# Kernel optimization log

Hardware: AMD Instinct MI355X
Metric: run time of the kernel (lower is better)

The kernel has to match this reference:

```python
import math
import jax, jax.numpy as jnp
import numpy as np

B, LQ, LK = 4, 128, 512
EMBED_TIME, NUM_HEADS, INPUT_DIM, HIDDEN_DIM = 128, 8, 64, 256
EK = EMBED_TIME // NUM_HEADS  # per-head time-embedding dim


def setup_inputs() -> dict:
    key = jax.random.key(0)
    ks = jax.random.split(key, 10)
    query = jax.random.normal(ks[0], (B, LQ, EMBED_TIME), dtype=jnp.float32)
    k_in = jax.random.normal(ks[1], (B, LK, EMBED_TIME), dtype=jnp.float32)
    value = jax.random.normal(ks[2], (B, LK, INPUT_DIM), dtype=jnp.float32)
    mask = jax.random.randint(ks[3], (B, LK, INPUT_DIM), 0, 2, dtype=jnp.int32)
    s_t = 1.0 / math.sqrt(EMBED_TIME)
    s_o = 1.0 / math.sqrt(NUM_HEADS * INPUT_DIM)
    Wq = jax.random.normal(ks[4], (EMBED_TIME, EMBED_TIME), dtype=jnp.float32) * s_t
    bq = jnp.zeros((EMBED_TIME,), dtype=jnp.float32)
    Wk = jax.random.normal(ks[5], (EMBED_TIME, EMBED_TIME), dtype=jnp.float32) * s_t
    bk = jnp.zeros((EMBED_TIME,), dtype=jnp.float32)
    Wo = jax.random.normal(ks[6], (NUM_HEADS * INPUT_DIM, HIDDEN_DIM), dtype=jnp.float32) * s_o
    bo = jnp.zeros((HIDDEN_DIM,), dtype=jnp.float32)
    return {"query": query, "key": k_in, "value": value, "mask": mask,
            "Wq": Wq, "bq": bq, "Wk": Wk, "bk": bk, "Wo": Wo, "bo": bo}


def reference(query, key, value, mask, Wq, bq, Wk, bk, Wo, bo):
    b, lq, _ = query.shape
    lk = key.shape[1]
    d = value.shape[-1]
    # project and split heads: [B, L, embed_time] -> [B, H, L, ek]
    q = (query @ Wq + bq).reshape(b, lq, NUM_HEADS, EK).transpose(0, 2, 1, 3)
    k = (key @ Wk + bk).reshape(b, lk, NUM_HEADS, EK).transpose(0, 2, 1, 3)
    # raw scores [B, H, Lq, Lk]
    scores = jnp.einsum("bhqe,bhke->bhqk", q, k) / math.sqrt(EK)
    # broadcast over value feature dim D and apply per-(time, feature) mask:
    # scores[..., None] -> [B,H,Lq,Lk,1], mask -> [B,1,1,Lk,D]
    m = mask[:, None, None, :, :]  # int 0/1
    scores_bd = jnp.where(m == 0, jnp.float32(-10000.0),
                          scores[..., None])  # [B,H,Lq,Lk,D]
    attn = jax.nn.softmax(scores_bd, axis=-2)  # softmax over Lk per feature
    # weighted sum over Lk with value [B,1,1,Lk,D] -> context [B,H,Lq,D]
    context = jnp.sum(attn * value[:, None, None, :, :], axis=-2)
    # merge heads: [B, Lq, H*D] and output projection
    context = context.transpose(0, 2, 1, 3).reshape(b, lq, NUM_HEADS * d)
    return context @ Wo + bo
```

## Files before the change

kernel.cpp:

```cpp
#include <hip/hip_runtime.h>
#include <math.h>

#define NB 4
#define LQ 128
#define LK 512
#define ET 128
#define NH 8
#define EKD 16
#define DD 64
#define HD 256

#define QP_OFF 0
#define KPB_OFF (NB*LQ*ET)
#define CTX_OFF (KPB_OFF + NB*NH*LK*EKD)

#define QS_B 10240
#define ES_B 10496

__global__ __launch_bounds__(256) void proj_kernel(
    const float* __restrict__ query, const float* __restrict__ key,
    const float* __restrict__ Wq, const float* __restrict__ bq,
    const float* __restrict__ Wk, const float* __restrict__ bk,
    float* __restrict__ ws)
{
  __shared__ float Xs[16][132];
  const int blk = blockIdx.x;
  const int tid = threadIdx.x;
  const bool isQ = (blk < 32);
  const float* X; const float* W; const float* bias; int rowbase;
  if (isQ) { X = query; W = Wq; bias = bq; rowbase = blk * 16; }
  else     { X = key;   W = Wk; bias = bk; rowbase = (blk - 32) * 16; }

  for (int idx = tid; idx < 16 * 32; idx += 256) {
    int r = idx >> 5, c4 = idx & 31;
    *(float4*)(&Xs[r][c4 * 4]) = ((const float4*)(X + (size_t)(rowbase + r) * ET))[c4];
  }
  __syncthreads();

  const int r  = tid >> 4;
  const int c0 = (tid & 15) * 8;
  float acc[8] = {0.f,0.f,0.f,0.f,0.f,0.f,0.f,0.f};
  #pragma unroll 8
  for (int kk = 0; kk < ET; ++kk) {
    float x = Xs[r][kk];
    const float* wrow = W + (size_t)kk * ET + c0;
    float4 w0 = *(const float4*)(wrow);
    float4 w1 = *(const float4*)(wrow + 4);
    acc[0] = fmaf(x, w0.x, acc[0]);
    acc[1] = fmaf(x, w0.y, acc[1]);
    acc[2] = fmaf(x, w0.z, acc[2]);
    acc[3] = fmaf(x, w0.w, acc[3]);
    acc[4] = fmaf(x, w1.x, acc[4]);
    acc[5] = fmaf(x, w1.y, acc[5]);
    acc[6] = fmaf(x, w1.z, acc[6]);
    acc[7] = fmaf(x, w1.w, acc[7]);
  }
  float4 bb0 = *(const float4*)(bias + c0);
  float4 bb1 = *(const float4*)(bias + c0 + 4);
  float4 o0 = make_float4(acc[0]+bb0.x, acc[1]+bb0.y, acc[2]+bb0.z, acc[3]+bb0.w);
  float4 o1 = make_float4(acc[4]+bb1.x, acc[5]+bb1.y, acc[6]+bb1.z, acc[7]+bb1.w);

  if (isQ) {
    float* orow = ws + QP_OFF + (size_t)(rowbase + r) * ET + c0;
    *(float4*)(orow)     = o0;
    *(float4*)(orow + 4) = o1;
  } else {
    const int row  = rowbase + r;
    const int b    = row >> 9;
    const int krow = row & 511;
    const int h    = c0 >> 4;
    const int cin  = c0 & 15;
    float* dst = ws + KPB_OFF + ((size_t)(b * NH + h) * LK + krow) * EKD + cin;
    *(float4*)(dst)     = o0;
    *(float4*)(dst + 4) = o1;
  }
}

__global__ __launch_bounds__(256) void attn_kernel(
    const float* __restrict__ value, const int* __restrict__ mask,
    float* __restrict__ ws)
{
  __shared__ __align__(16) float S[14656];
  const int bx  = blockIdx.x;
  const int tid = threadIdx.x;
  const int b  = bx >> 7;
  const int h  = (bx >> 4) & 7;
  const int qt = bx & 15;

  const float* Qp = ws + QP_OFF;
  const float* Kb = ws + KPB_OFF + (size_t)(b * NH + h) * LK * EKD;
  float* ctx = ws + CTX_OFF;

  for (int idx = tid; idx < 2048; idx += 256) {
    int k = idx >> 2, j4 = idx & 3;
    float4 v4 = *(const float4*)(Kb + (size_t)idx * 4);
    *(float4*)(&S[k * 20 + j4 * 4]) = v4;
  }
  if (tid < 32) {
    int r = tid >> 2, j4 = tid & 3;
    *(float4*)(&S[QS_B + r * 16 + j4 * 4]) =
        *(const float4*)(Qp + (size_t)(b * LQ + qt * 8 + r) * ET + h * EKD + j4 * 4);
  }
  __syncthreads();

  {
    const int r = tid >> 5;
    const int i = tid & 31;
    float qreg[16];
    #pragma unroll
    for (int j = 0; j < 16; ++j) qreg[j] = S[QS_B + r * 16 + j];

    float sv[16];
    float smax = -1e30f;
    #pragma unroll 4
    for (int kk = 0; kk < 16; ++kk) {
      int k = kk * 32 + i;
      const float* kp = &S[k * 20];
      float4 k0 = *(const float4*)(kp);
      float4 k1 = *(const float4*)(kp + 4);
      float4 k2 = *(const float4*)(kp + 8);
      float4 k3 = *(const float4*)(kp + 12);
      float dot = qreg[0] * k0.x;
      dot = fmaf(qreg[1],  k0.y, dot);
      dot = fmaf(qreg[2],  k0.z, dot);
      dot = fmaf(qreg[3],  k0.w, dot);
      dot = fmaf(qreg[4],  k1.x, dot);
      dot = fmaf(qreg[5],  k1.y, dot);
      dot = fmaf(qreg[6],  k1.z, dot);
      dot = fmaf(qreg[7],  k1.w, dot);
      dot = fmaf(qreg[8],  k2.x, dot);
      dot = fmaf(qreg[9],  k2.y, dot);
      dot = fmaf(qreg[10], k2.z, dot);
      dot = fmaf(qreg[11], k2.w, dot);
      dot = fmaf(qreg[12], k3.x, dot);
      dot = fmaf(qreg[13], k3.y, dot);
      dot = fmaf(qreg[14], k3.z, dot);
      dot = fmaf(qreg[15], k3.w, dot);
      float s = dot * 0.25f;
      sv[kk] = s;
      smax = fmaxf(smax, s);
    }
    #pragma unroll
    for (int off = 1; off < 32; off <<= 1)
      smax = fmaxf(smax, __shfl_xor(smax, off));
    #pragma unroll
    for (int kk = 0; kk < 16; ++kk)
      S[ES_B + r * 520 + kk * 32 + i] = __expf(sv[kk] - smax);
  }
  __syncthreads();

  {
    const int w = tid >> 6;
    const int d = tid & 63;
    float num[8], den[8];
    #pragma unroll
    for (int r = 0; r < 8; ++r) { num[r] = 0.f; den[r] = 0.f; }

    const int*   mcol = mask  + (size_t)b * LK * DD + d;
    const float* vcol = value + (size_t)b * LK * DD + d;
    const int kbase = w * 128;

    #pragma unroll 4
    for (int kb = 0; kb < 32; ++kb) {
      const int k = kbase + kb * 4;
      float m0 = (float)mcol[(size_t)(k + 0) * DD];
      float m1 = (float)mcol[(size_t)(k + 1) * DD];
      float m2 = (float)mcol[(size_t)(k + 2) * DD];
      float m3 = (float)mcol[(size_t)(k + 3) * DD];
      float v0 = vcol[(size_t)(k + 0) * DD];
      float v1 = vcol[(size_t)(k + 1) * DD];
      float v2 = vcol[(size_t)(k + 2) * DD];
      float v3 = vcol[(size_t)(k + 3) * DD];
      float mv0 = m0 * v0, mv1 = m1 * v1, mv2 = m2 * v2, mv3 = m3 * v3;
      #pragma unroll
      for (int r = 0; r < 8; ++r) {
        float4 e = *(const float4*)(&S[ES_B + r * 520 + k]);
        num[r] = fmaf(e.x, mv0, num[r]);
        num[r] = fmaf(e.y, mv1, num[r]);
        num[r] = fmaf(e.z, mv2, num[r]);
        num[r] = fmaf(e.w, mv3, num[r]);
        den[r] = fmaf(e.x, m0, den[r]);
        den[r] = fmaf(e.y, m1, den[r]);
        den[r] = fmaf(e.z, m2, den[r]);
        den[r] = fmaf(e.w, m3, den[r]);
      }
    }
    #pragma unroll
    for (int r = 0; r < 8; ++r) {
      S[(w * 8 + r) * 64 + d]        = num[r];
      S[2048 + (w * 8 + r) * 64 + d] = den[r];
    }
  }
  __syncthreads();

  {
    const int d  = tid & 63;
    const int rg = tid >> 6;
    #pragma unroll
    for (int j = 0; j < 2; ++j) {
      const int r = rg * 2 + j;
      float n  = S[(r) * 64 + d]        + S[(8 + r) * 64 + d]
               + S[(16 + r) * 64 + d]   + S[(24 + r) * 64 + d];
      float dn = S[2048 + (r) * 64 + d] + S[2048 + (8 + r) * 64 + d]
               + S[2048 + (16 + r) * 64 + d] + S[2048 + (24 + r) * 64 + d];
      const int row = b * LQ + qt * 8 + r;
      ctx[(size_t)row * (NH * DD) + h * DD + d] = n / dn;
    }
  }
}

__global__ __launch_bounds__(256) void outproj_kernel(
    const float* __restrict__ Wo, const float* __restrict__ bo,
    const float* __restrict__ ws, float* __restrict__ out)
{
  __shared__ __align__(16) float S[10304];
  const float* ctx = ws + CTX_OFF;
  const int bx = blockIdx.x;
  const int rt = bx >> 3;
  const int ct = bx & 7;
  const int r0 = rt * 16, c0 = ct * 32;
  const int tid = threadIdx.x;

  for (int idx = tid; idx < 16 * 128; idx += 256) {
    int r = idx >> 7, c4 = idx & 127;
    *(float4*)(&S[r * 516 + c4 * 4]) =
        *(const float4*)(ctx + (size_t)(r0 + r) * 512 + c4 * 4);
  }
  __syncthreads();

  const int w    = tid >> 6;
  const int lane = tid & 63;
  const int rh   = lane >> 5;
  const int cc   = lane & 31;
  const int c    = c0 + cc;
  float acc[8];
  #pragma unroll
  for (int r = 0; r < 8; ++r) acc[r] = 0.f;

  const int kbase = w * 128;
  #pragma unroll 4
  for (int kb = 0; kb < 32; ++kb) {
    const int k = kbase + kb * 4;
    float w0 = Wo[(size_t)(k + 0) * HD + c];
    float w1 = Wo[(size_t)(k + 1) * HD + c];
    float w2 = Wo[(size_t)(k + 2) * HD + c];
    float w3 = Wo[(size_t)(k + 3) * HD + c];
    #pragma unroll
    for (int r = 0; r < 8; ++r) {
      const int row = rh * 8 + r;
      float4 cs = *(const float4*)(&S[row * 516 + k]);
      acc[r] = fmaf(cs.x, w0, acc[r]);
      acc[r] = fmaf(cs.y, w1, acc[r]);
      acc[r] = fmaf(cs.z, w2, acc[r]);
      acc[r] = fmaf(cs.w, w3, acc[r]);
    }
  }
  #pragma unroll
  for (int r = 0; r < 8; ++r)
    S[8256 + ((size_t)w * 16 + rh * 8 + r) * 32 + cc] = acc[r];
  __syncthreads();

  {
    const int row = tid >> 4;
    const int cc0 = (tid & 15) * 2;
    #pragma unroll
    for (int j = 0; j < 2; ++j) {
      const int ccj = cc0 + j;
      float s = S[8256 + (0 * 16 + row) * 32 + ccj]
              + S[8256 + (1 * 16 + row) * 32 + ccj]
              + S[8256 + (2 * 16 + row) * 32 + ccj]
              + S[8256 + (3 * 16 + row) * 32 + ccj];
      out[(size_t)(r0 + row) * HD + c0 + ccj] = s + bo[c0 + ccj];
    }
  }
}

extern "C" void kernel_launch(void* const* d_in, const int* in_sizes, int n_in,
                              void* d_out, int out_size, void* d_ws, size_t ws_size,
                              hipStream_t stream) {
  const float* query = (const float*)d_in[0];
  const float* key   = (const float*)d_in[1];
  const float* value = (const float*)d_in[2];
  const int*   mask  = (const int*)d_in[3];
  const float* Wq    = (const float*)d_in[4];
  const float* bq    = (const float*)d_in[5];
  const float* Wk    = (const float*)d_in[6];
  const float* bk    = (const float*)d_in[7];
  const float* Wo    = (const float*)d_in[8];
  const float* bo    = (const float*)d_in[9];
  float* out = (float*)d_out;
  float* ws  = (float*)d_ws;

  proj_kernel<<<160, 256, 0, stream>>>(query, key, Wq, bq, Wk, bk, ws);
  attn_kernel<<<512, 256, 0, stream>>>(value, mask, ws);
  outproj_kernel<<<256, 256, 0, stream>>>(Wo, bo, ws, out);
}
```

Before: 114.0 us.

## Fuse output projection into attention kernel via per-head atomic accumulation

Removes the separate output-projection kernel. Each attention block now multiplies its 8x64 per-head context tile, kept in shared memory, by the matching 64-row slice of Wo and atomically adds the partial result into the output. The projection kernel gains extra blocks that pre-fill the output with the bias, and its tiles are halved to 8 rows so it runs more blocks. This drops one launch and the global round trip of the context tensor, at the cost of 8-way float atomics per output element and a result whose summation order is no longer fixed.

```diff
diff --git a/kernel.cpp b/kernel.cpp
--- a/kernel.cpp
+++ b/kernel.cpp
@@ -12,73 +12,75 @@
 
 #define QP_OFF 0
 #define KPB_OFF (NB*LQ*ET)
-#define CTX_OFF (KPB_OFF + NB*NH*LK*EKD)
 
 #define QS_B 10240
 #define ES_B 10496
+#define CTX_B 4096
 
 __global__ __launch_bounds__(256) void proj_kernel(
     const float* __restrict__ query, const float* __restrict__ key,
     const float* __restrict__ Wq, const float* __restrict__ bq,
     const float* __restrict__ Wk, const float* __restrict__ bk,
-    float* __restrict__ ws)
+    const float* __restrict__ bo,
+    float* __restrict__ ws, float* __restrict__ out)
 {
-  __shared__ float Xs[16][132];
   const int blk = blockIdx.x;
   const int tid = threadIdx.x;
-  const bool isQ = (blk < 32);
+
+  if (blk >= 320) {
+    const int bi = blk - 320;
+    for (int idx = tid; idx < 2048; idx += 256) {
+      const int r  = idx >> 6;
+      const int c4 = idx & 63;
+      float4 bb = *(const float4*)(bo + c4 * 4);
+      *(float4*)(out + (size_t)(bi * 32 + r) * HD + c4 * 4) = bb;
+    }
+    return;
+  }
+
+  __shared__ float Xs[8][132];
+  const bool isQ = (blk < 64);
   const float* X; const float* W; const float* bias; int rowbase;
-  if (isQ) { X = query; W = Wq; bias = bq; rowbase = blk * 16; }
-  else     { X = key;   W = Wk; bias = bk; rowbase = (blk - 32) * 16; }
-
-  for (int idx = tid; idx < 16 * 32; idx += 256) {
-    int r = idx >> 5, c4 = idx & 31;
+  if (isQ) { X = query; W = Wq; bias = bq; rowbase = blk * 8; }
+  else     { X = key;   W = Wk; bias = bk; rowbase = (blk - 64) * 8; }
+
+  {
+    const int r = tid >> 5, c4 = tid & 31;
     *(float4*)(&Xs[r][c4 * 4]) = ((const float4*)(X + (size_t)(rowbase + r) * ET))[c4];
   }
   __syncthreads();
 
-  const int r  = tid >> 4;
-  const int c0 = (tid & 15) * 8;
-  float acc[8] = {0.f,0.f,0.f,0.f,0.f,0.f,0.f,0.f};
+  const int r  = tid >> 5;
+  const int c0 = (tid & 31) * 4;
+  float acc[4] = {0.f, 0.f, 0.f, 0.f};
   #pragma unroll 8
   for (int kk = 0; kk < ET; ++kk) {
     float x = Xs[r][kk];
-    const float* wrow = W + (size_t)kk * ET + c0;
-    float4 w0 = *(const float4*)(wrow);
-    float4 w1 = *(const float4*)(wrow + 4);
-    acc[0] = fmaf(x, w0.x, acc[0]);
-    acc[1] = fmaf(x, w0.y, acc[1]);
-    acc[2] = fmaf(x, w0.z, acc[2]);
-    acc[3] = fmaf(x, w0.w, acc[3]);
-    acc[4] = fmaf(x, w1.x, acc[4]);
-    acc[5] = fmaf(x, w1.y, acc[5]);
-    acc[6] = fmaf(x, w1.z, acc[6]);
-    acc[7] = fmaf(x, w1.w, acc[7]);
-  }
-  float4 bb0 = *(const float4*)(bias + c0);
-  float4 bb1 = *(const float4*)(bias + c0 + 4);
-  float4 o0 = make_float4(acc[0]+bb0.x, acc[1]+bb0.y, acc[2]+bb0.z, acc[3]+bb0.w);
-  float4 o1 = make_float4(acc[4]+bb1.x, acc[5]+bb1.y, acc[6]+bb1.z, acc[7]+bb1.w);
+    float4 w = *(const float4*)(W + (size_t)kk * ET + c0);
+    acc[0] = fmaf(x, w.x, acc[0]);
+    acc[1] = fmaf(x, w.y, acc[1]);
+    acc[2] = fmaf(x, w.z, acc[2]);
+    acc[3] = fmaf(x, w.w, acc[3]);
+  }
+  float4 bb = *(const float4*)(bias + c0);
+  float4 o  = make_float4(acc[0]+bb.x, acc[1]+bb.y, acc[2]+bb.z, acc[3]+bb.w);
 
   if (isQ) {
-    float* orow = ws + QP_OFF + (size_t)(rowbase + r) * ET + c0;
-    *(float4*)(orow)     = o0;
-    *(float4*)(orow + 4) = o1;
+    *(float4*)(ws + QP_OFF + (size_t)(rowbase + r) * ET + c0) = o;
   } else {
     const int row  = rowbase + r;
     const int b    = row >> 9;
     const int krow = row & 511;
     const int h    = c0 >> 4;
     const int cin  = c0 & 15;
-    float* dst = ws + KPB_OFF + ((size_t)(b * NH + h) * LK + krow) * EKD + cin;
-    *(float4*)(dst)     = o0;
-    *(float4*)(dst + 4) = o1;
+    *(float4*)(ws + KPB_OFF + ((size_t)(b * NH + h) * LK + krow) * EKD + cin) = o;
   }
 }
 
 __global__ __launch_bounds__(256) void attn_kernel(
     const float* __restrict__ value, const int* __restrict__ mask,
-    float* __restrict__ ws)
+    const float* __restrict__ Wo,
+    const float* __restrict__ ws, float* __restrict__ out)
 {
   __shared__ __align__(16) float S[14656];
   const int bx  = blockIdx.x;
@@ -89,7 +91,6 @@
 
   const float* Qp = ws + QP_OFF;
   const float* Kb = ws + KPB_OFF + (size_t)(b * NH + h) * LK * EKD;
-  float* ctx = ws + CTX_OFF;
 
   for (int idx = tid; idx < 2048; idx += 256) {
     int k = idx >> 2, j4 = idx & 3;
@@ -203,75 +204,38 @@
                + S[(16 + r) * 64 + d]   + S[(24 + r) * 64 + d];
       float dn = S[2048 + (r) * 64 + d] + S[2048 + (8 + r) * 64 + d]
                + S[2048 + (16 + r) * 64 + d] + S[2048 + (24 + r) * 64 + d];
-      const int row = b * LQ + qt * 8 + r;
-      ctx[(size_t)row * (NH * DD) + h * DD + d] = n / dn;
-    }
-  }
-}
-
-__global__ __launch_bounds__(256) void outproj_kernel(
-    const float* __restrict__ Wo, const float* __restrict__ bo,
-    const float* __restrict__ ws, float* __restrict__ out)
-{
-  __shared__ __align__(16) float S[10304];
-  const float* ctx = ws + CTX_OFF;
-  const int bx = blockIdx.x;
-  const int rt = bx >> 3;
-  const int ct = bx & 7;
-  const int r0 = rt * 16, c0 = ct * 32;
-  const int tid = threadIdx.x;
-
-  for (int idx = tid; idx < 16 * 128; idx += 256) {
-    int r = idx >> 7, c4 = idx & 127;
-    *(float4*)(&S[r * 516 + c4 * 4]) =
-        *(const float4*)(ctx + (size_t)(r0 + r) * 512 + c4 * 4);
-  }
-  __syncthreads();
-
-  const int w    = tid >> 6;
-  const int lane = tid & 63;
-  const int rh   = lane >> 5;
-  const int cc   = lane & 31;
-  const int c    = c0 + cc;
-  float acc[8];
-  #pragma unroll
-  for (int r = 0; r < 8; ++r) acc[r] = 0.f;
-
-  const int kbase = w * 128;
-  #pragma unroll 4
-  for (int kb = 0; kb < 32; ++kb) {
-    const int k = kbase + kb * 4;
-    float w0 = Wo[(size_t)(k + 0) * HD + c];
-    float w1 = Wo[(size_t)(k + 1) * HD + c];
-    float w2 = Wo[(size_t)(k + 2) * HD + c];
-    float w3 = Wo[(size_t)(k + 3) * HD + c];
-    #pragma unroll
-    for (int r = 0; r < 8; ++r) {
-      const int row = rh * 8 + r;
-      float4 cs = *(const float4*)(&S[row * 516 + k]);
-      acc[r] = fmaf(cs.x, w0, acc[r]);
-      acc[r] = fmaf(cs.y, w1, acc[r]);
-      acc[r] = fmaf(cs.z, w2, acc[r]);
-      acc[r] = fmaf(cs.w, w3, acc[r]);
-    }
-  }
-  #pragma unroll
-  for (int r = 0; r < 8; ++r)
-    S[8256 + ((size_t)w * 16 + rh * 8 + r) * 32 + cc] = acc[r];
-  __syncthreads();
-
-  {
-    const int row = tid >> 4;
-    const int cc0 = (tid & 15) * 2;
-    #pragma unroll
-    for (int j = 0; j < 2; ++j) {
-      const int ccj = cc0 + j;
-      float s = S[8256 + (0 * 16 + row) * 32 + ccj]
-              + S[8256 + (1 * 16 + row) * 32 + ccj]
-              + S[8256 + (2 * 16 + row) * 32 + ccj]
-              + S[8256 + (3 * 16 + row) * 32 + ccj];
-      out[(size_t)(r0 + row) * HD + c0 + ccj] = s + bo[c0 + ccj];
-    }
+      S[CTX_B + r * 68 + d] = n / dn;
+    }
+  }
+  __syncthreads();
+
+  {
+    const int c = tid;
+    const float* wocol = Wo + (size_t)(h * DD) * HD + c;
+    float acc[8];
+    #pragma unroll
+    for (int r = 0; r < 8; ++r) acc[r] = 0.f;
+
+    #pragma unroll 4
+    for (int d4 = 0; d4 < 16; ++d4) {
+      const int d = d4 * 4;
+      float w0 = wocol[(size_t)(d + 0) * HD];
+      float w1 = wocol[(size_t)(d + 1) * HD];
+      float w2 = wocol[(size_t)(d + 2) * HD];
+      float w3 = wocol[(size_t)(d + 3) * HD];
+      #pragma unroll
+      for (int r = 0; r < 8; ++r) {
+        float4 e = *(const float4*)(&S[CTX_B + r * 68 + d]);
+        acc[r] = fmaf(e.x, w0, acc[r]);
+        acc[r] = fmaf(e.y, w1, acc[r]);
+        acc[r] = fmaf(e.z, w2, acc[r]);
+        acc[r] = fmaf(e.w, w3, acc[r]);
+      }
+    }
+    const int row0 = b * LQ + qt * 8;
+    #pragma unroll
+    for (int r = 0; r < 8; ++r)
+      atomicAdd(out + (size_t)(row0 + r) * HD + c, acc[r]);
   }
 }
 
@@ -291,7 +255,6 @@
   float* out = (float*)d_out;
   float* ws  = (float*)d_ws;
 
-  proj_kernel<<<160, 256, 0, stream>>>(query, key, Wq, bq, Wk, bk, ws);
-  attn_kernel<<<512, 256, 0, stream>>>(value, mask, ws);
-  outproj_kernel<<<256, 256, 0, stream>>>(Wo, bo, ws, out);
+  proj_kernel<<<336, 256, 0, stream>>>(query, key, Wq, bq, Wk, bk, bo, ws, out);
+  attn_kernel<<<512, 256, 0, stream>>>(value, mask, Wo, ws, out);
 }
```

After: 100.7 us. 1.13x faster.
